# Kernel optimization log

Hardware: AMD Instinct MI355X
Metric: run time of the kernel (lower is better)

The kernel has to match this reference:

```python
import jax, jax.numpy as jnp
from jax import lax
import numpy as np

D_MODEL = 768
D_STATE = 16
D_CONV = 4
EXPAND = 2
D_INNER = EXPAND * D_MODEL
BATCH = 2
SEQ = 512


def setup_inputs() -> dict:
    key = jax.random.key(0)
    ks = jax.random.split(key, 8)
    s = 0.02
    return {
        "x": jax.random.normal(ks[0], (BATCH, SEQ, D_MODEL), jnp.float32),
        "W_in": jax.random.normal(ks[1], (2 * D_INNER, D_MODEL), jnp.float32) * s,
        "conv_w": jax.random.normal(ks[2], (D_INNER, 1, D_CONV), jnp.float32) * s,
        "conv_b": jnp.zeros((D_INNER,), jnp.float32),
        "W_x": jax.random.normal(ks[3], (D_INNER + 2 * D_STATE, D_INNER), jnp.float32) * s,
        "W_dt": jax.random.normal(ks[4], (D_INNER, D_INNER), jnp.float32) * s,
        "b_dt": jnp.zeros((D_INNER,), jnp.float32),
        "A_log": jnp.log(jax.random.uniform(ks[5], (D_INNER, D_STATE), jnp.float32, 1e-4, 1.0)),
        "Dp": jnp.ones((D_INNER,), jnp.float32),
        "W_out": jax.random.normal(ks[6], (D_MODEL, D_INNER), jnp.float32) * s,
    }


def parallel_scan_log(log_coeffs, log_values):
    """Faithful port of ParallelScan.parallel_scan_log (Blelchh-style up/down sweep
    in log space). Indices are static, so the Python loop over O(log L) levels is
    trace-time only."""
    B, L, D = log_coeffs.shape
    if L <= 4:
        run = log_values[:, 0]
        outs = [run]
        for i in range(1, L):
            run = jnp.logaddexp(run, log_coeffs[:, i] + log_values[:, i])
            outs.append(run)
        return jnp.stack(outs, axis=1)
    levels = int(np.ceil(np.log2(L)))
    coeffs, values = log_coeffs, log_values
    # up-sweep
    for level in range(levels):
        step = 2 ** (level + 1)
        if step - 1 >= L:
            break
        right = np.arange(step - 1, L, step)
        left = right - 2 ** level
        m = (left >= 0) & (right < L)
        left, right = left[m], right[m]
        if left.size == 0:
            continue
        new_c = coeffs[:, left] + coeffs[:, right]
        new_v = jnp.logaddexp(values[:, left], coeffs[:, right] + values[:, right])
        coeffs = coeffs.at[:, right].set(new_c)
        values = values.at[:, right].set(new_v)
    # down-sweep
    for level in range(levels - 1, -1, -1):
        step = 2 ** (level + 1)
        if step - 1 >= L:
            continue
        right = np.arange(step - 1, L, step)
        left = right - 2 ** level
        m = (left >= 0) & (right < L)
        left, right = left[m], right[m]
        if left.size == 0:
            continue
        tmp = values[:, right]
        new_r = jnp.logaddexp(values[:, left], coeffs[:, right] + values[:, right])
        values = values.at[:, right].set(new_r)
        values = values.at[:, left].set(tmp)
    return values


def reference(x, W_in, conv_w, conv_b, W_x, W_dt, b_dt, A_log, Dp, W_out):
    Bsz, L, _ = x.shape
    xz = x @ W_in.T                                 # [B, L, 2*d_inner]
    x_inner, z = jnp.split(xz, 2, axis=-1)
    # depthwise causal conv1d (pad left d_conv-1, truncate to L == torch slice)
    xc = jnp.transpose(x_inner, (0, 2, 1))          # [B, d_inner, L]
    xc = lax.conv_general_dilated(
        xc, conv_w, (1,), [(D_CONV - 1, 0)],
        dimension_numbers=("NCH", "OIH", "NCH"),
        feature_group_count=D_INNER)
    xc = xc + conv_b[None, :, None]
    x_conv = jax.nn.silu(jnp.transpose(xc, (0, 2, 1)))  # [B, L, d_inner]
    x_dbl = x_conv @ W_x.T                              # [B, L, d_inner + 2*d_state]
    delta, Bmat, Cmat = jnp.split(x_dbl, [D_INNER, D_INNER + D_STATE], axis=-1)
    delta = jax.nn.softplus(delta @ W_dt.T + b_dt)      # [B, L, d_inner]
    # selective scan
    A = -jnp.exp(A_log)                                 # [d_inner, d_state]
    deltaA = jnp.exp(jnp.einsum("bld,dn->bldn", delta, A))
    deltaB_u = jnp.einsum("bld,bln,bld->bldn", delta, Bmat, x_conv)
    log_coeffs = jnp.log(deltaA + 1e-12).reshape(Bsz, L, -1)
    log_values = jnp.log(jnp.abs(deltaB_u) + 1e-12).reshape(Bsz, L, -1)
    scanned = jnp.exp(parallel_scan_log(log_coeffs, log_values))
    scanned = scanned.reshape(Bsz, L, D_INNER, D_STATE)
    y = jnp.einsum("bldn,bln->bld", scanned, Cmat) + x_conv * Dp
    y = y * jax.nn.silu(z)
    return y @ W_out.T
```

## Files before the change

kernel.cpp:

```cpp
#include <hip/hip_runtime.h>
#include <math.h>

#define D_MODEL 768
#define D_STATE 16
#define D_CONV  4
#define D_INNER 1536
#define BATCH   2
#define SEQ     512
#define M_ROWS  (BATCH * SEQ)
#define N_XZ    (2 * D_INNER)
#define N_XDBL  (D_INNER + 2 * D_STATE)

typedef _Float16 half8 __attribute__((ext_vector_type(8)));
typedef float  f32x4  __attribute__((ext_vector_type(4)));
typedef unsigned short ushort_t;
typedef ushort_t ushort8_t __attribute__((ext_vector_type(8)));

__device__ __forceinline__ ushort_t f2h(float f) {
    _Float16 h = (_Float16)f;
    return *(ushort_t*)&h;
}
__device__ __forceinline__ void pack8(const float* s, ushort_t* d) {
    ushort8_t o;
#pragma unroll
    for (int j = 0; j < 8; ++j) o[j] = f2h(s[j]);
    *(ushort8_t*)d = o;
}
__device__ __forceinline__ void gld16(const ushort_t* g, void* l) {
    __builtin_amdgcn_global_load_lds((const __attribute__((address_space(1))) void*)g,
                                     (__attribute__((address_space(3))) void*)l, 16, 0, 0);
}

#define SX  (M_ROWS * D_MODEL)
#define SW1 (N_XZ * D_MODEL)
#define SW2 (N_XDBL * D_INNER)
__global__ __launch_bounds__(256) void split3_kernel(
    const float* __restrict__ x, const float* __restrict__ win,
    const float* __restrict__ wx,
    ushort_t* __restrict__ xs, ushort_t* __restrict__ w1, ushort_t* __restrict__ w2)
{
    long i = ((long)blockIdx.x * 256 + threadIdx.x) * 8;
    const float* src; ushort_t* dst; long base;
    if (i < SX)            { src = x;   dst = xs; base = i; }
    else if (i < SX + SW1) { src = win; dst = w1; base = i - SX; }
    else                   { src = wx;  dst = w2; base = i - SX - SW1; }
    float v[8];
    *(float4*)(v)     = *(const float4*)(src + base);
    *(float4*)(v + 4) = *(const float4*)(src + base + 4);
    pack8(v, dst + base);
}

#define SWDT (D_INNER * D_INNER)
#define SWO  (D_MODEL * D_INNER)
__global__ __launch_bounds__(256) void split2_kernel(
    const float* __restrict__ wdt, const float* __restrict__ wo,
    ushort_t* __restrict__ w1, ushort_t* __restrict__ wout)
{
    long i = ((long)blockIdx.x * 256 + threadIdx.x) * 8;
    const float* src; ushort_t* dst; long base;
    if (i < SWDT) { src = wdt; dst = w1;   base = i; }
    else          { src = wo;  dst = wout; base = i - SWDT; }
    float v[8];
    *(float4*)(v)     = *(const float4*)(src + base);
    *(float4*)(v + 4) = *(const float4*)(src + base + 4);
    pack8(v, dst + base);
}

__global__ __launch_bounds__(256) void gemm_lds(
    const ushort_t* __restrict__ A, int lda,
    const ushort_t* __restrict__ B, int ldb,
    float* __restrict__ Cbase, long pstride, int ldc,
    int N, int kc)
{
    __shared__ ushort_t smA[2][4096];
    __shared__ ushort_t smB[2][4096];

    const int tid  = threadIdx.x;
    const int w    = tid >> 6;
    const int lane = tid & 63;
    const int lr   = lane & 15;
    const int lq   = lane >> 4;

    const int Gx = gridDim.x, Gy = gridDim.y;
    const int T = Gx * Gy * gridDim.z;
    const int f = blockIdx.x + Gx * (blockIdx.y + Gy * blockIdx.z);
    const int g = (T & 7) ? f : ((f & 7) * (T >> 3) + (f >> 3));
    const int bx = g % Gx;
    const int by = (g / Gx) % Gy;
    const int z  = g / (Gx * Gy);
    float* __restrict__ C = Cbase + (long)z * pstride;

    const int bm = by * 128;
    const int bn = bx * 128;
    const int k0base = z * kc;

    auto stage = [&](int buf, int k0) {
#pragma unroll
        for (int i = 0; i < 2; ++i) {
            const int gA = i * 4 + w;
            const int rA = bm + gA * 16 + lr;
            gld16(A + (long)rA * lda + k0 + lq * 8, &smA[buf][gA * 512]);
        }
#pragma unroll
        for (int i = 0; i < 2; ++i) {
            const int gB = i * 4 + w;
            int rB = bn + gB * 16 + lr; if (rB >= N) rB = N - 1;
            gld16(B + (long)rB * ldb + k0 + lq * 8, &smB[buf][gB * 512]);
        }
    };

    f32x4 acc[4][4] = {};
    const int wm = (w & 1) * 64;
    const int wn = (w >> 1) * 64;

    stage(0, k0base);
    __syncthreads();
    const int nIter = kc >> 5;
    for (int it = 0; it < nIter; ++it) {
        const int buf = it & 1;
        if (it + 1 < nIter) stage(buf ^ 1, k0base + (it + 1) * 32);

        half8 ah[4], bh[4];
#pragma unroll
        for (int mt = 0; mt < 4; ++mt)
            ah[mt] = *(const half8*)&smA[buf][(((w & 1) * 4 + mt) * 512) + lq * 128 + lr * 8];
#pragma unroll
        for (int nt = 0; nt < 4; ++nt)
            bh[nt] = *(const half8*)&smB[buf][(((w >> 1) * 4 + nt) * 512) + lq * 128 + lr * 8];
#pragma unroll
        for (int mt = 0; mt < 4; ++mt)
#pragma unroll
            for (int nt = 0; nt < 4; ++nt)
                acc[mt][nt] = __builtin_amdgcn_mfma_f32_16x16x32_f16(ah[mt], bh[nt], acc[mt][nt], 0, 0, 0);
        __syncthreads();
    }

#pragma unroll
    for (int mt = 0; mt < 4; ++mt)
#pragma unroll
        for (int nt = 0; nt < 4; ++nt)
#pragma unroll
            for (int r = 0; r < 4; ++r) {
                int row = bm + wm + mt * 16 + lq * 4 + r;
                int col = bn + wn + nt * 16 + lr;
                if (col >= N) continue;
                C[(long)row * ldc + col] = acc[mt][nt][r];
            }
}

__global__ __launch_bounds__(256) void conv_silu_kernel(
    const float* __restrict__ p0, const float* __restrict__ p1,
    const float* __restrict__ conv_w,
    const float* __restrict__ conv_b,
    float* __restrict__ xconvT,
    float* __restrict__ zsiluT,
    ushort_t* __restrict__ xc)
{
    int idx = blockIdx.x * blockDim.x + threadIdx.x;
    if (idx >= M_ROWS * D_INNER) return;
    int d = idx % D_INNER;
    int r = idx / D_INNER;
    int l = r % SEQ;
    float acc = conv_b[d];
#pragma unroll
    for (int k = 0; k < D_CONV; ++k) {
        if (l - (D_CONV - 1) + k >= 0) {
            long o = (long)(r - (D_CONV - 1 - k)) * N_XZ + d;
            acc = fmaf(conv_w[d * D_CONV + k], p0[o] + p1[o], acc);
        }
    }
    float s = acc / (1.f + expf(-acc));
    xconvT[(long)d * M_ROWS + r] = s;
    xc[(long)r * D_INNER + d] = f2h(s);
    long oz = (long)r * N_XZ + D_INNER + d;
    float zv = p0[oz] + p1[oz];
    zsiluT[(long)d * M_ROWS + r] = zv / (1.f + expf(-zv));
}

__global__ __launch_bounds__(256) void ep_xdbl_kernel(
    const float* __restrict__ P, long ps,
    ushort_t* __restrict__ xd, float* __restrict__ BCT)
{
    long i = ((long)blockIdx.x * 256 + threadIdx.x) * 8;
    if (i >= (long)M_ROWS * N_XDBL) return;
    int row = (int)(i / N_XDBL);
    int col = (int)(i - (long)row * N_XDBL);
    float f[8];
#pragma unroll
    for (int j = 0; j < 8; ++j) f[j] = P[i + j] + P[i + j + ps] + P[i + j + 2 * ps];
    pack8(f, xd + i);
    if (col >= D_INNER) {
#pragma unroll
        for (int j = 0; j < 8; ++j)
            BCT[(long)(col + j - D_INNER) * M_ROWS + row] = f[j];
    }
}

__global__ __launch_bounds__(256) void ep_merge_kernel(
    const float* __restrict__ P, long ps, float* __restrict__ out)
{
    long i = ((long)blockIdx.x * 256 + threadIdx.x) * 8;
    if (i >= (long)M_ROWS * D_MODEL) return;
    float o[8];
#pragma unroll
    for (int j = 0; j < 8; ++j) {
        float v = 0.f;
#pragma unroll
        for (int z = 0; z < 6; ++z) v += P[i + j + z * ps];
        o[j] = v;
    }
    *(float4*)(out + i)     = *(float4*)(o);
    *(float4*)(out + i + 4) = *(float4*)(o + 4);
}

__global__ __launch_bounds__(256) void scan_kernel(
    const float* __restrict__ P, long ps,
    const float* __restrict__ b_dt,
    const float* __restrict__ xconvT,
    const float* __restrict__ zsiluT,
    const float* __restrict__ BCT,
    const float* __restrict__ A_log,
    const float* __restrict__ Dp,
    float* __restrict__ uT)
{
    __shared__ float dlT[512];
    __shared__ float xrT[512];
    __shared__ float red[3 * 512];

    const int bid = blockIdx.x;
    const int b   = bid / D_INNER;
    const int d   = bid % D_INNER;
    const int tid = threadIdx.x;
    const int w   = tid >> 6;
    const int t   = tid & 63;
    const long od = (long)d * M_ROWS + b * SEQ;

    const float bdt = b_dt[d];
#pragma unroll
    for (int q = 0; q < 2; ++q) {
        const int l = tid + q * 256;
        float v = P[od + l] + P[od + l + ps] + P[od + l + 2 * ps] + P[od + l + 3 * ps] + bdt;
        float sp = fmaxf(v, 0.f) + log1pf(expf(-fabsf(v)));
        const int li = (l & 7) * 64 + (l >> 3);
        dlT[li] = sp;
        xrT[li] = xconvT[od + l];
    }
    __syncthreads();

    float dl[8], xr[8], dx[8], yac[8];
#pragma unroll
    for (int j = 0; j < 8; ++j) {
        dl[j] = dlT[j * 64 + t];
        xr[j] = xrT[j * 64 + t];
        dx[j] = dl[j] * xr[j];
        yac[j] = 0.f;
    }
    const int l0 = 8 * t;

#pragma unroll
    for (int nn = 0; nn < 4; ++nn) {
        const int n = w * 4 + nn;
        const float Adn = -expf(A_log[d * D_STATE + n]);
        const float4* Bp = (const float4*)(BCT + (long)n * M_ROWS + b * SEQ + l0);
        float4 b0 = Bp[0], b1 = Bp[1];
        float Bv[8] = {b0.x, b0.y, b0.z, b0.w, b1.x, b1.y, b1.z, b1.w};
        float c[8], v[8];
#pragma unroll
        for (int j = 0; j < 8; ++j) {
            c[j] = __expf(dl[j] * Adn);
            v[j] = fabsf(dx[j] * Bv[j]);
        }
        float c01 = c[1] * c[0], v01 = fmaf(c[1], v[0], v[1]);
        float c23 = c[3] * c[2], v23 = fmaf(c[3], v[2], v[3]);
        float c45 = c[5] * c[4], v45 = fmaf(c[5], v[4], v[5]);
        float c67 = c[7] * c[6], v67 = fmaf(c[7], v[6], v[7]);
        float c03 = c23 * c01,  v03 = fmaf(c23, v01, v23);
        float c47 = c67 * c45,  v47 = fmaf(c67, v45, v67);
        float cA  = c47 * c03,  vA  = fmaf(c47, v03, v47);
#pragma unroll
        for (int h = 1; h <= 32; h <<= 1) {
            float cl = __shfl_up(cA, (unsigned)h);
            float vl = __shfl_up(vA, (unsigned)h);
            if (t >= h) { vA = fmaf(cA, vl, vA); cA = cA * cl; }
        }
        float s = __shfl_up(vA, 1u);
        if (t == 0) s = 0.f;
        const float4* Cp = (const float4*)(BCT + (long)(16 + n) * M_ROWS + b * SEQ + l0);
        float4 c0 = Cp[0], c1 = Cp[1];
        float Cv[8] = {c0.x, c0.y, c0.z, c0.w, c1.x, c1.y, c1.z, c1.w};
#pragma unroll
        for (int j = 0; j < 8; ++j) {
            s = fmaf(c[j], s, v[j]);
            yac[j] = fmaf(s, Cv[j], yac[j]);
        }
    }

    if (w) {
#pragma unroll
        for (int j = 0; j < 8; ++j) red[(w - 1) * 512 + j * 64 + t] = yac[j];
    }
    __syncthreads();
    if (w == 0) {
        const float Dpd = Dp[d];
#pragma unroll
        for (int j = 0; j < 8; ++j) {
            float y = yac[j] + red[j * 64 + t] + red[512 + j * 64 + t] + red[1024 + j * 64 + t];
            float uv = fmaf(xr[j], Dpd, y) * zsiluT[od + l0 + j];
            uT[od + l0 + j] = uv;
        }
    }
}

__global__ __launch_bounds__(256) void transpose_split_kernel(
    const float* __restrict__ uT, ushort_t* __restrict__ u)
{
    __shared__ float T[64][65];
    const int m0 = blockIdx.x * 64;
    const int d0 = blockIdx.y * 64;
    const int c  = threadIdx.x & 63;
    const int rr = threadIdx.x >> 6;
#pragma unroll
    for (int p = 0; p < 64; p += 4)
        T[p + rr][c] = uT[(long)(d0 + p + rr) * M_ROWS + m0 + c];
    __syncthreads();
#pragma unroll
    for (int p = 0; p < 64; p += 4) {
        int rm = p + rr;
        float v = T[c][rm];
        u[(long)(m0 + rm) * D_INNER + (d0 + c)] = f2h(v);
    }
}

extern "C" void kernel_launch(void* const* d_in, const int* in_sizes, int n_in,
                              void* d_out, int out_size, void* d_ws, size_t ws_size,
                              hipStream_t stream)
{
    (void)in_sizes; (void)n_in; (void)out_size; (void)ws_size;

    const float* x      = (const float*)d_in[0];
    const float* W_in   = (const float*)d_in[1];
    const float* conv_w = (const float*)d_in[2];
    const float* conv_b = (const float*)d_in[3];
    const float* W_x    = (const float*)d_in[4];
    const float* W_dt   = (const float*)d_in[5];
    const float* b_dt   = (const float*)d_in[6];
    const float* A_log  = (const float*)d_in[7];
    const float* Dp     = (const float*)d_in[8];
    const float* W_out  = (const float*)d_in[9];
    float* out = (float*)d_out;

    float* ws = (float*)d_ws;
    long off = 0;
    float* P      = ws + off; off += 2L * M_ROWS * N_XZ;
    float* xconvT = ws + off; off += (long)D_INNER * M_ROWS;
    float* zsiluT = ws + off; off += (long)D_INNER * M_ROWS;
    float* uT     = ws + off; off += (long)D_INNER * M_ROWS;
    float* xcu    = ws + off; off += (long)M_ROWS * D_INNER / 2;
    float* xsbuf  = ws + off; off += (long)M_ROWS * D_MODEL / 2;
    float* w1buf  = ws + off; off += (long)N_XZ * D_MODEL / 2;
    float* w2buf  = ws + off; off += (long)N_XDBL * D_INNER / 2;
    float* xdbuf  = ws + off; off += (long)M_ROWS * N_XDBL / 2;
    float* BCT    = ws + off; off += (long)2 * D_STATE * M_ROWS;

    ushort_t* xs   = (ushort_t*)xsbuf;
    ushort_t* w1   = (ushort_t*)w1buf;
    ushort_t* w2   = (ushort_t*)w2buf;
    ushort_t* xc   = (ushort_t*)xcu;
    ushort_t* xd   = (ushort_t*)xdbuf;
    ushort_t* u_i  = (ushort_t*)xcu;
    float* P6      = P;

    const long psG4 = (long)D_INNER * M_ROWS;

    dim3 blk(256);

    hipLaunchKernelGGL(split3_kernel, dim3((SX + SW1 + SW2) / 2048), blk, 0, stream,
                       x, W_in, W_x, xs, w1, w2);
    hipLaunchKernelGGL(gemm_lds, dim3(N_XZ / 128, M_ROWS / 128, 2), blk, 0, stream,
                       xs, D_MODEL, w1, D_MODEL,
                       P, (long)M_ROWS * N_XZ, N_XZ, N_XZ, D_MODEL / 2);
    hipLaunchKernelGGL(conv_silu_kernel, dim3((M_ROWS * D_INNER) / 256), blk, 0, stream,
                       P, P + (long)M_ROWS * N_XZ, conv_w, conv_b, xconvT, zsiluT, xc);
    hipLaunchKernelGGL(gemm_lds, dim3((N_XDBL + 127) / 128, M_ROWS / 128, 3), blk, 0, stream,
                       xc, D_INNER, w2, D_INNER,
                       P, (long)M_ROWS * N_XDBL, N_XDBL, N_XDBL, D_INNER / 3);
    hipLaunchKernelGGL(ep_xdbl_kernel, dim3((M_ROWS * N_XDBL) / 2048), blk, 0, stream,
                       P, (long)M_ROWS * N_XDBL, xd, BCT);
    hipLaunchKernelGGL(split2_kernel, dim3((SWDT + SWO) / 2048), blk, 0, stream,
                       W_dt, W_out, w1, w2);
    hipLaunchKernelGGL(gemm_lds, dim3(M_ROWS / 128, D_INNER / 128, 4), blk, 0, stream,
                       w1, D_INNER, xd, N_XDBL,
                       P, psG4, M_ROWS, M_ROWS, D_INNER / 4);
    hipLaunchKernelGGL(scan_kernel, dim3(BATCH * D_INNER), blk, 0, stream,
                       P, psG4, b_dt, xconvT, zsiluT, BCT, A_log, Dp, uT);
    hipLaunchKernelGGL(transpose_split_kernel, dim3(M_ROWS / 64, D_INNER / 64), blk, 0, stream,
                       uT, u_i);
    hipLaunchKernelGGL(gemm_lds, dim3(D_MODEL / 128, M_ROWS / 128, 6), blk, 0, stream,
                       u_i, D_INNER, w2, D_INNER,
                       P6, (long)M_ROWS * D_MODEL, D_MODEL, D_MODEL, D_INNER / 6);
    hipLaunchKernelGGL(ep_merge_kernel, dim3((M_ROWS * D_MODEL) / 2048), blk, 0, stream,
                       P6, (long)M_ROWS * D_MODEL, out);
}
```

Baseline: 223.1 us.

## Replace split-K GEMMs with smaller-tile full-K GEMMs and fused epilogues

Drops split-K partial-sum buffers and the separate reduction kernels. Each GEMM now uses 64-row tiles over the full K, and the x_dbl GEMM writes half-precision delta and the transposed B/C directly from its epilogue. The two weight-packing kernels become one launch, and the conv/silu kernel is tiled so the transposed stores go through shared memory and are coalesced. This saves global traffic and launches, but the GEMMs may have fewer waves in flight and longer per-block K loops.

```diff
diff --git a/kernel.cpp b/kernel.cpp
--- a/kernel.cpp
+++ b/kernel.cpp
@@ -31,49 +31,45 @@
                                      (__attribute__((address_space(3))) void*)l, 16, 0, 0);
 }
 
-#define SX  (M_ROWS * D_MODEL)
-#define SW1 (N_XZ * D_MODEL)
-#define SW2 (N_XDBL * D_INNER)
-__global__ __launch_bounds__(256) void split3_kernel(
+#define SX   (M_ROWS * D_MODEL)
+#define SW1  (N_XZ * D_MODEL)
+#define SW2  (N_XDBL * D_INNER)
+#define SWDT (D_INNER * D_INNER)
+#define SWO  (D_MODEL * D_INNER)
+#define SPACK (SX + SW1 + SW2 + SWDT + SWO)
+__global__ __launch_bounds__(256) void pack_kernel(
     const float* __restrict__ x, const float* __restrict__ win,
-    const float* __restrict__ wx,
-    ushort_t* __restrict__ xs, ushort_t* __restrict__ w1, ushort_t* __restrict__ w2)
+    const float* __restrict__ wx, const float* __restrict__ wdt,
+    const float* __restrict__ wo,
+    ushort_t* __restrict__ xs, ushort_t* __restrict__ w1, ushort_t* __restrict__ w2,
+    ushort_t* __restrict__ wdt16, ushort_t* __restrict__ wo16)
 {
     long i = ((long)blockIdx.x * 256 + threadIdx.x) * 8;
+    if (i >= SPACK) return;
     const float* src; ushort_t* dst; long base;
-    if (i < SX)            { src = x;   dst = xs; base = i; }
-    else if (i < SX + SW1) { src = win; dst = w1; base = i - SX; }
-    else                   { src = wx;  dst = w2; base = i - SX - SW1; }
+    if (i < SX)                         { src = x;   dst = xs;    base = i; }
+    else if (i < SX + SW1)              { src = win; dst = w1;    base = i - SX; }
+    else if (i < SX + SW1 + SW2)        { src = wx;  dst = w2;    base = i - SX - SW1; }
+    else if (i < SX + SW1 + SW2 + SWDT) { src = wdt; dst = wdt16; base = i - SX - SW1 - SW2; }
+    else                                { src = wo;  dst = wo16;  base = i - SX - SW1 - SW2 - SWDT; }
     float v[8];
     *(float4*)(v)     = *(const float4*)(src + base);
     *(float4*)(v + 4) = *(const float4*)(src + base + 4);
     pack8(v, dst + base);
 }
 
-#define SWDT (D_INNER * D_INNER)
-#define SWO  (D_MODEL * D_INNER)
-__global__ __launch_bounds__(256) void split2_kernel(
-    const float* __restrict__ wdt, const float* __restrict__ wo,
-    ushort_t* __restrict__ w1, ushort_t* __restrict__ wout)
-{
-    long i = ((long)blockIdx.x * 256 + threadIdx.x) * 8;
-    const float* src; ushort_t* dst; long base;
-    if (i < SWDT) { src = wdt; dst = w1;   base = i; }
-    else          { src = wo;  dst = wout; base = i - SWDT; }
-    float v[8];
-    *(float4*)(v)     = *(const float4*)(src + base);
-    *(float4*)(v + 4) = *(const float4*)(src + base + 4);
-    pack8(v, dst + base);
-}
-
-__global__ __launch_bounds__(256) void gemm_lds(
+template<int BN, int EPI>
+__global__ __launch_bounds__(256) void gemm_z1(
     const ushort_t* __restrict__ A, int lda,
     const ushort_t* __restrict__ B, int ldb,
-    float* __restrict__ Cbase, long pstride, int ldc,
-    int N, int kc)
-{
-    __shared__ ushort_t smA[2][4096];
-    __shared__ ushort_t smB[2][4096];
+    float* __restrict__ C, int ldc,
+    int N, int K,
+    ushort_t* __restrict__ Ch, float* __restrict__ BCT)
+{
+    constexpr int FN = BN / 32;
+    constexpr int BG = BN / 16;
+    __shared__ ushort_t smA[2][2048];
+    __shared__ ushort_t smB[2][BN * 32];
 
     const int tid  = threadIdx.x;
     const int w    = tid >> 6;
@@ -81,140 +77,118 @@
     const int lr   = lane & 15;
     const int lq   = lane >> 4;
 
-    const int Gx = gridDim.x, Gy = gridDim.y;
-    const int T = Gx * Gy * gridDim.z;
-    const int f = blockIdx.x + Gx * (blockIdx.y + Gy * blockIdx.z);
+    const int Gx = gridDim.x;
+    const int T = Gx * gridDim.y;
+    const int f = blockIdx.x + Gx * blockIdx.y;
     const int g = (T & 7) ? f : ((f & 7) * (T >> 3) + (f >> 3));
     const int bx = g % Gx;
-    const int by = (g / Gx) % Gy;
-    const int z  = g / (Gx * Gy);
-    float* __restrict__ C = Cbase + (long)z * pstride;
-
-    const int bm = by * 128;
-    const int bn = bx * 128;
-    const int k0base = z * kc;
+    const int by = g / Gx;
+    const int bm = by * 64;
+    const int bn = bx * BN;
 
     auto stage = [&](int buf, int k0) {
-#pragma unroll
-        for (int i = 0; i < 2; ++i) {
-            const int gA = i * 4 + w;
-            const int rA = bm + gA * 16 + lr;
-            gld16(A + (long)rA * lda + k0 + lq * 8, &smA[buf][gA * 512]);
-        }
-#pragma unroll
-        for (int i = 0; i < 2; ++i) {
+        {
+            const int rA = bm + w * 16 + lr;
+            gld16(A + (long)rA * lda + k0 + lq * 8, &smA[buf][w * 512]);
+        }
+#pragma unroll
+        for (int i = 0; i < BG / 4; ++i) {
             const int gB = i * 4 + w;
             int rB = bn + gB * 16 + lr; if (rB >= N) rB = N - 1;
             gld16(B + (long)rB * ldb + k0 + lq * 8, &smB[buf][gB * 512]);
         }
     };
 
-    f32x4 acc[4][4] = {};
-    const int wm = (w & 1) * 64;
-    const int wn = (w >> 1) * 64;
-
-    stage(0, k0base);
-    __syncthreads();
-    const int nIter = kc >> 5;
+    f32x4 acc[2][FN] = {};
+    const int wm = (w & 1) * 32;
+    const int wn = (w >> 1) * (BN / 2);
+
+    stage(0, 0);
+    __syncthreads();
+    const int nIter = K >> 5;
     for (int it = 0; it < nIter; ++it) {
         const int buf = it & 1;
-        if (it + 1 < nIter) stage(buf ^ 1, k0base + (it + 1) * 32);
-
-        half8 ah[4], bh[4];
-#pragma unroll
-        for (int mt = 0; mt < 4; ++mt)
-            ah[mt] = *(const half8*)&smA[buf][(((w & 1) * 4 + mt) * 512) + lq * 128 + lr * 8];
-#pragma unroll
-        for (int nt = 0; nt < 4; ++nt)
-            bh[nt] = *(const half8*)&smB[buf][(((w >> 1) * 4 + nt) * 512) + lq * 128 + lr * 8];
-#pragma unroll
-        for (int mt = 0; mt < 4; ++mt)
-#pragma unroll
-            for (int nt = 0; nt < 4; ++nt)
+        if (it + 1 < nIter) stage(buf ^ 1, (it + 1) * 32);
+
+        half8 ah[2], bh[FN];
+#pragma unroll
+        for (int mt = 0; mt < 2; ++mt)
+            ah[mt] = *(const half8*)&smA[buf][(((w & 1) * 2 + mt) * 512) + lq * 128 + lr * 8];
+#pragma unroll
+        for (int nt = 0; nt < FN; ++nt)
+            bh[nt] = *(const half8*)&smB[buf][(((w >> 1) * FN + nt) * 512) + lq * 128 + lr * 8];
+#pragma unroll
+        for (int mt = 0; mt < 2; ++mt)
+#pragma unroll
+            for (int nt = 0; nt < FN; ++nt)
                 acc[mt][nt] = __builtin_amdgcn_mfma_f32_16x16x32_f16(ah[mt], bh[nt], acc[mt][nt], 0, 0, 0);
         __syncthreads();
     }
 
 #pragma unroll
-    for (int mt = 0; mt < 4; ++mt)
-#pragma unroll
-        for (int nt = 0; nt < 4; ++nt)
+    for (int mt = 0; mt < 2; ++mt)
+#pragma unroll
+        for (int nt = 0; nt < FN; ++nt)
 #pragma unroll
             for (int r = 0; r < 4; ++r) {
                 int row = bm + wm + mt * 16 + lq * 4 + r;
                 int col = bn + wn + nt * 16 + lr;
-                if (col >= N) continue;
-                C[(long)row * ldc + col] = acc[mt][nt][r];
+                if (EPI == 0) {
+                    if (col < N) C[(long)row * ldc + col] = acc[mt][nt][r];
+                } else {
+                    if (col < D_INNER)
+                        Ch[(long)row * D_INNER + col] = f2h(acc[mt][nt][r]);
+                    else if (col < N)
+                        BCT[(long)(col - D_INNER) * M_ROWS + row] = acc[mt][nt][r];
+                }
             }
 }
 
 __global__ __launch_bounds__(256) void conv_silu_kernel(
-    const float* __restrict__ p0, const float* __restrict__ p1,
-    const float* __restrict__ conv_w,
-    const float* __restrict__ conv_b,
-    float* __restrict__ xconvT,
-    float* __restrict__ zsiluT,
+    const float* __restrict__ xz,
+    const float* __restrict__ conv_w, const float* __restrict__ conv_b,
+    float* __restrict__ xconvT, float* __restrict__ zsiluT,
     ushort_t* __restrict__ xc)
 {
-    int idx = blockIdx.x * blockDim.x + threadIdx.x;
-    if (idx >= M_ROWS * D_INNER) return;
-    int d = idx % D_INNER;
-    int r = idx / D_INNER;
-    int l = r % SEQ;
-    float acc = conv_b[d];
-#pragma unroll
-    for (int k = 0; k < D_CONV; ++k) {
-        if (l - (D_CONV - 1) + k >= 0) {
-            long o = (long)(r - (D_CONV - 1 - k)) * N_XZ + d;
-            acc = fmaf(conv_w[d * D_CONV + k], p0[o] + p1[o], acc);
-        }
-    }
-    float s = acc / (1.f + expf(-acc));
-    xconvT[(long)d * M_ROWS + r] = s;
-    xc[(long)r * D_INNER + d] = f2h(s);
-    long oz = (long)r * N_XZ + D_INNER + d;
-    float zv = p0[oz] + p1[oz];
-    zsiluT[(long)d * M_ROWS + r] = zv / (1.f + expf(-zv));
-}
-
-__global__ __launch_bounds__(256) void ep_xdbl_kernel(
-    const float* __restrict__ P, long ps,
-    ushort_t* __restrict__ xd, float* __restrict__ BCT)
-{
-    long i = ((long)blockIdx.x * 256 + threadIdx.x) * 8;
-    if (i >= (long)M_ROWS * N_XDBL) return;
-    int row = (int)(i / N_XDBL);
-    int col = (int)(i - (long)row * N_XDBL);
-    float f[8];
-#pragma unroll
-    for (int j = 0; j < 8; ++j) f[j] = P[i + j] + P[i + j + ps] + P[i + j + 2 * ps];
-    pack8(f, xd + i);
-    if (col >= D_INNER) {
-#pragma unroll
-        for (int j = 0; j < 8; ++j)
-            BCT[(long)(col + j - D_INNER) * M_ROWS + row] = f[j];
-    }
-}
-
-__global__ __launch_bounds__(256) void ep_merge_kernel(
-    const float* __restrict__ P, long ps, float* __restrict__ out)
-{
-    long i = ((long)blockIdx.x * 256 + threadIdx.x) * 8;
-    if (i >= (long)M_ROWS * D_MODEL) return;
-    float o[8];
-#pragma unroll
-    for (int j = 0; j < 8; ++j) {
-        float v = 0.f;
-#pragma unroll
-        for (int z = 0; z < 6; ++z) v += P[i + j + z * ps];
-        o[j] = v;
-    }
-    *(float4*)(out + i)     = *(float4*)(o);
-    *(float4*)(out + i + 4) = *(float4*)(o + 4);
+    __shared__ float Tx[64][17];
+    __shared__ float Tz[64][17];
+    const int rb = blockIdx.x;
+    const int db = blockIdx.y;
+    const int dl = threadIdx.x & 63;
+    const int d  = db * 64 + dl;
+    const int rr = threadIdx.x >> 6;
+    const float w0 = conv_w[d * 4 + 0], w1 = conv_w[d * 4 + 1];
+    const float w2 = conv_w[d * 4 + 2], w3 = conv_w[d * 4 + 3];
+    const float bb = conv_b[d];
+#pragma unroll
+    for (int q = 0; q < 4; ++q) {
+        const int r = rb * 16 + q * 4 + rr;
+        const int l = r & (SEQ - 1);
+        float acc = bb;
+        if (l >= 3) acc = fmaf(w0, xz[(long)(r - 3) * N_XZ + d], acc);
+        if (l >= 2) acc = fmaf(w1, xz[(long)(r - 2) * N_XZ + d], acc);
+        if (l >= 1) acc = fmaf(w2, xz[(long)(r - 1) * N_XZ + d], acc);
+        acc = fmaf(w3, xz[(long)r * N_XZ + d], acc);
+        float s = acc / (1.f + expf(-acc));
+        xc[(long)r * D_INNER + d] = f2h(s);
+        float zv = xz[(long)r * N_XZ + D_INNER + d];
+        Tx[dl][q * 4 + rr] = s;
+        Tz[dl][q * 4 + rr] = zv / (1.f + expf(-zv));
+    }
+    __syncthreads();
+    const int rp = threadIdx.x & 15;
+    const int dp = threadIdx.x >> 4;
+#pragma unroll
+    for (int p = 0; p < 4; ++p) {
+        int dd = p * 16 + dp;
+        long o = (long)(db * 64 + dd) * M_ROWS + rb * 16 + rp;
+        xconvT[o] = Tx[dd][rp];
+        zsiluT[o] = Tz[dd][rp];
+    }
 }
 
 __global__ __launch_bounds__(256) void scan_kernel(
-    const float* __restrict__ P, long ps,
+    const float* __restrict__ dpre,
     const float* __restrict__ b_dt,
     const float* __restrict__ xconvT,
     const float* __restrict__ zsiluT,
@@ -239,7 +213,7 @@
 #pragma unroll
     for (int q = 0; q < 2; ++q) {
         const int l = tid + q * 256;
-        float v = P[od + l] + P[od + l + ps] + P[od + l + 2 * ps] + P[od + l + 3 * ps] + bdt;
+        float v = dpre[od + l] + bdt;
         float sp = fmaxf(v, 0.f) + log1pf(expf(-fabsf(v)));
         const int li = (l & 7) * 64 + (l >> 3);
         dlT[li] = sp;
@@ -351,53 +325,46 @@
 
     float* ws = (float*)d_ws;
     long off = 0;
-    float* P      = ws + off; off += 2L * M_ROWS * N_XZ;
+    float* xzbuf  = ws + off; off += (long)M_ROWS * N_XZ;
     float* xconvT = ws + off; off += (long)D_INNER * M_ROWS;
     float* zsiluT = ws + off; off += (long)D_INNER * M_ROWS;
     float* uT     = ws + off; off += (long)D_INNER * M_ROWS;
-    float* xcu    = ws + off; off += (long)M_ROWS * D_INNER / 2;
+    float* xcbuf  = ws + off; off += (long)M_ROWS * D_INNER / 2;
+    float* xdbuf  = ws + off; off += (long)M_ROWS * D_INNER / 2;
     float* xsbuf  = ws + off; off += (long)M_ROWS * D_MODEL / 2;
     float* w1buf  = ws + off; off += (long)N_XZ * D_MODEL / 2;
     float* w2buf  = ws + off; off += (long)N_XDBL * D_INNER / 2;
-    float* xdbuf  = ws + off; off += (long)M_ROWS * N_XDBL / 2;
+    float* wdtbuf = ws + off; off += (long)D_INNER * D_INNER / 2;
+    float* wobuf  = ws + off; off += (long)D_MODEL * D_INNER / 2;
     float* BCT    = ws + off; off += (long)2 * D_STATE * M_ROWS;
 
-    ushort_t* xs   = (ushort_t*)xsbuf;
-    ushort_t* w1   = (ushort_t*)w1buf;
-    ushort_t* w2   = (ushort_t*)w2buf;
-    ushort_t* xc   = (ushort_t*)xcu;
-    ushort_t* xd   = (ushort_t*)xdbuf;
-    ushort_t* u_i  = (ushort_t*)xcu;
-    float* P6      = P;
-
-    const long psG4 = (long)D_INNER * M_ROWS;
+    ushort_t* xs    = (ushort_t*)xsbuf;
+    ushort_t* w1    = (ushort_t*)w1buf;
+    ushort_t* w2    = (ushort_t*)w2buf;
+    ushort_t* wdt16 = (ushort_t*)wdtbuf;
+    ushort_t* wo16  = (ushort_t*)wobuf;
+    ushort_t* xc    = (ushort_t*)xcbuf;
+    ushort_t* xd    = (ushort_t*)xdbuf;
+    ushort_t* u_i   = (ushort_t*)xcbuf;
+    float* xz       = xzbuf;
+    float* dpreT    = xzbuf;
 
     dim3 blk(256);
 
-    hipLaunchKernelGGL(split3_kernel, dim3((SX + SW1 + SW2) / 2048), blk, 0, stream,
-                       x, W_in, W_x, xs, w1, w2);
-    hipLaunchKernelGGL(gemm_lds, dim3(N_XZ / 128, M_ROWS / 128, 2), blk, 0, stream,
-                       xs, D_MODEL, w1, D_MODEL,
-                       P, (long)M_ROWS * N_XZ, N_XZ, N_XZ, D_MODEL / 2);
-    hipLaunchKernelGGL(conv_silu_kernel, dim3((M_ROWS * D_INNER) / 256), blk, 0, stream,
-                       P, P + (long)M_ROWS * N_XZ, conv_w, conv_b, xconvT, zsiluT, xc);
-    hipLaunchKernelGGL(gemm_lds, dim3((N_XDBL + 127) / 128, M_ROWS / 128, 3), blk, 0, stream,
-                       xc, D_INNER, w2, D_INNER,
-                       P, (long)M_ROWS * N_XDBL, N_XDBL, N_XDBL, D_INNER / 3);
-    hipLaunchKernelGGL(ep_xdbl_kernel, dim3((M_ROWS * N_XDBL) / 2048), blk, 0, stream,
-                       P, (long)M_ROWS * N_XDBL, xd, BCT);
-    hipLaunchKernelGGL(split2_kernel, dim3((SWDT + SWO) / 2048), blk, 0, stream,
-                       W_dt, W_out, w1, w2);
-    hipLaunchKernelGGL(gemm_lds, dim3(M_ROWS / 128, D_INNER / 128, 4), blk, 0, stream,
-                       w1, D_INNER, xd, N_XDBL,
-                       P, psG4, M_ROWS, M_ROWS, D_INNER / 4);
-    hipLaunchKernelGGL(scan_kernel, dim3(BATCH * D_INNER), blk, 0, stream,
-                       P, psG4, b_dt, xconvT, zsiluT, BCT, A_log, Dp, uT);
-    hipLaunchKernelGGL(transpose_split_kernel, dim3(M_ROWS / 64, D_INNER / 64), blk, 0, stream,
-                       uT, u_i);
-    hipLaunchKernelGGL(gemm_lds, dim3(D_MODEL / 128, M_ROWS / 128, 6), blk, 0, stream,
-                       u_i, D_INNER, w2, D_INNER,
-                       P6, (long)M_ROWS * D_MODEL, D_MODEL, D_MODEL, D_INNER / 6);
-    hipLaunchKernelGGL(ep_merge_kernel, dim3((M_ROWS * D_MODEL) / 2048), blk, 0, stream,
-                       P6, (long)M_ROWS * D_MODEL, out);
-}
+    pack_kernel<<<dim3(SPACK / 2048), blk, 0, stream>>>(
+        x, W_in, W_x, W_dt, W_out, xs, w1, w2, wdt16, wo16);
+    gemm_z1<128, 0><<<dim3(N_XZ / 128, M_ROWS / 64), blk, 0, stream>>>(
+        xs, D_MODEL, w1, D_MODEL, xz, N_XZ, N_XZ, D_MODEL, nullptr, nullptr);
+    conv_silu_kernel<<<dim3(M_ROWS / 16, D_INNER / 64), blk, 0, stream>>>(
+        xz, conv_w, conv_b, xconvT, zsiluT, xc);
+    gemm_z1<64, 1><<<dim3((N_XDBL + 63) / 64, M_ROWS / 64), blk, 0, stream>>>(
+        xc, D_INNER, w2, D_INNER, nullptr, 0, N_XDBL, D_INNER, xd, BCT);
+    gemm_z1<64, 0><<<dim3(M_ROWS / 64, D_INNER / 64), blk, 0, stream>>>(
+        wdt16, D_INNER, xd, D_INNER, dpreT, M_ROWS, M_ROWS, D_INNER, nullptr, nullptr);
+    scan_kernel<<<dim3(BATCH * D_INNER), blk, 0, stream>>>(
+        dpreT, b_dt, xconvT, zsiluT, BCT, A_log, Dp, uT);
+    transpose_split_kernel<<<dim3(M_ROWS / 64, D_INNER / 64), blk, 0, stream>>>(
+        uT, u_i);
+    gemm_z1<64, 0><<<dim3(D_MODEL / 64, M_ROWS / 64), blk, 0, stream>>>(
+        u_i, D_INNER, wo16, D_INNER, out, D_MODEL, D_MODEL, D_INNER, nullptr, nullptr);
+}
```

Result: no change. 227.4 us (+1.9%).

## Triple-buffer GEMM LDS pipeline, merge weight packing, tile-transpose conv output

Applied to the files above, without the earlier changes.

The GEMM moves from double to triple LDS buffering. The trailing __syncthreads per iteration becomes one barrier per iteration, preceded by a partial vmcnt wait, so the next tile's global-to-LDS loads stay in flight during the MFMA work. The two fp16 packing kernels become one launch with separate buffers for W_dt and W_out. The conv+SiLU kernel now transposes through shared-memory tiles so its transposed outputs are written coalesced instead of strided. The costs are more LDS per block, which may lower occupancy, and a fragile hand-written waitcnt scheme.

```diff
diff --git a/kernel.cpp b/kernel.cpp
--- a/kernel.cpp
+++ b/kernel.cpp
@@ -31,35 +31,27 @@
                                      (__attribute__((address_space(3))) void*)l, 16, 0, 0);
 }
 
-#define SX  (M_ROWS * D_MODEL)
-#define SW1 (N_XZ * D_MODEL)
-#define SW2 (N_XDBL * D_INNER)
-__global__ __launch_bounds__(256) void split3_kernel(
-    const float* __restrict__ x, const float* __restrict__ win,
-    const float* __restrict__ wx,
-    ushort_t* __restrict__ xs, ushort_t* __restrict__ w1, ushort_t* __restrict__ w2)
-{
-    long i = ((long)blockIdx.x * 256 + threadIdx.x) * 8;
-    const float* src; ushort_t* dst; long base;
-    if (i < SX)            { src = x;   dst = xs; base = i; }
-    else if (i < SX + SW1) { src = win; dst = w1; base = i - SX; }
-    else                   { src = wx;  dst = w2; base = i - SX - SW1; }
-    float v[8];
-    *(float4*)(v)     = *(const float4*)(src + base);
-    *(float4*)(v + 4) = *(const float4*)(src + base + 4);
-    pack8(v, dst + base);
-}
-
+#define SX   (M_ROWS * D_MODEL)
+#define SW1  (N_XZ * D_MODEL)
+#define SW2  (N_XDBL * D_INNER)
 #define SWDT (D_INNER * D_INNER)
 #define SWO  (D_MODEL * D_INNER)
-__global__ __launch_bounds__(256) void split2_kernel(
-    const float* __restrict__ wdt, const float* __restrict__ wo,
-    ushort_t* __restrict__ w1, ushort_t* __restrict__ wout)
+#define SPACK (SX + SW1 + SW2 + SWDT + SWO)
+__global__ __launch_bounds__(256) void pack_kernel(
+    const float* __restrict__ x, const float* __restrict__ win,
+    const float* __restrict__ wx, const float* __restrict__ wdt,
+    const float* __restrict__ wo,
+    ushort_t* __restrict__ xs, ushort_t* __restrict__ w1, ushort_t* __restrict__ w2,
+    ushort_t* __restrict__ wdt16, ushort_t* __restrict__ wo16)
 {
     long i = ((long)blockIdx.x * 256 + threadIdx.x) * 8;
+    if (i >= SPACK) return;
     const float* src; ushort_t* dst; long base;
-    if (i < SWDT) { src = wdt; dst = w1;   base = i; }
-    else          { src = wo;  dst = wout; base = i - SWDT; }
+    if (i < SX)                         { src = x;   dst = xs;    base = i; }
+    else if (i < SX + SW1)              { src = win; dst = w1;    base = i - SX; }
+    else if (i < SX + SW1 + SW2)        { src = wx;  dst = w2;    base = i - SX - SW1; }
+    else if (i < SX + SW1 + SW2 + SWDT) { src = wdt; dst = wdt16; base = i - SX - SW1 - SW2; }
+    else                                { src = wo;  dst = wo16;  base = i - SX - SW1 - SW2 - SWDT; }
     float v[8];
     *(float4*)(v)     = *(const float4*)(src + base);
     *(float4*)(v + 4) = *(const float4*)(src + base + 4);
@@ -72,8 +64,8 @@
     float* __restrict__ Cbase, long pstride, int ldc,
     int N, int kc)
 {
-    __shared__ ushort_t smA[2][4096];
-    __shared__ ushort_t smB[2][4096];
+    __shared__ ushort_t smA[3][4096];
+    __shared__ ushort_t smB[3][4096];
 
     const int tid  = threadIdx.x;
     const int w    = tid >> 6;
@@ -114,25 +106,32 @@
     const int wn = (w >> 1) * 64;
 
     stage(0, k0base);
-    __syncthreads();
     const int nIter = kc >> 5;
+    int cur = 0;
     for (int it = 0; it < nIter; ++it) {
-        const int buf = it & 1;
-        if (it + 1 < nIter) stage(buf ^ 1, k0base + (it + 1) * 32);
+        const int nxt = (cur == 2) ? 0 : cur + 1;
+        if (it + 1 < nIter) {
+            stage(nxt, k0base + (it + 1) * 32);
+            asm volatile("s_waitcnt vmcnt(4)" ::: "memory");
+        } else {
+            asm volatile("s_waitcnt vmcnt(0)" ::: "memory");
+        }
+        __builtin_amdgcn_s_barrier();
+        asm volatile("" ::: "memory");
 
         half8 ah[4], bh[4];
 #pragma unroll
         for (int mt = 0; mt < 4; ++mt)
-            ah[mt] = *(const half8*)&smA[buf][(((w & 1) * 4 + mt) * 512) + lq * 128 + lr * 8];
+            ah[mt] = *(const half8*)&smA[cur][(((w & 1) * 4 + mt) * 512) + lq * 128 + lr * 8];
 #pragma unroll
         for (int nt = 0; nt < 4; ++nt)
-            bh[nt] = *(const half8*)&smB[buf][(((w >> 1) * 4 + nt) * 512) + lq * 128 + lr * 8];
+            bh[nt] = *(const half8*)&smB[cur][(((w >> 1) * 4 + nt) * 512) + lq * 128 + lr * 8];
 #pragma unroll
         for (int mt = 0; mt < 4; ++mt)
 #pragma unroll
             for (int nt = 0; nt < 4; ++nt)
                 acc[mt][nt] = __builtin_amdgcn_mfma_f32_16x16x32_f16(ah[mt], bh[nt], acc[mt][nt], 0, 0, 0);
-        __syncthreads();
+        cur = nxt;
     }
 
 #pragma unroll
@@ -150,31 +149,46 @@
 
 __global__ __launch_bounds__(256) void conv_silu_kernel(
     const float* __restrict__ p0, const float* __restrict__ p1,
-    const float* __restrict__ conv_w,
-    const float* __restrict__ conv_b,
-    float* __restrict__ xconvT,
-    float* __restrict__ zsiluT,
+    const float* __restrict__ conv_w, const float* __restrict__ conv_b,
+    float* __restrict__ xconvT, float* __restrict__ zsiluT,
     ushort_t* __restrict__ xc)
 {
-    int idx = blockIdx.x * blockDim.x + threadIdx.x;
-    if (idx >= M_ROWS * D_INNER) return;
-    int d = idx % D_INNER;
-    int r = idx / D_INNER;
-    int l = r % SEQ;
-    float acc = conv_b[d];
-#pragma unroll
-    for (int k = 0; k < D_CONV; ++k) {
-        if (l - (D_CONV - 1) + k >= 0) {
-            long o = (long)(r - (D_CONV - 1 - k)) * N_XZ + d;
-            acc = fmaf(conv_w[d * D_CONV + k], p0[o] + p1[o], acc);
-        }
-    }
-    float s = acc / (1.f + expf(-acc));
-    xconvT[(long)d * M_ROWS + r] = s;
-    xc[(long)r * D_INNER + d] = f2h(s);
-    long oz = (long)r * N_XZ + D_INNER + d;
-    float zv = p0[oz] + p1[oz];
-    zsiluT[(long)d * M_ROWS + r] = zv / (1.f + expf(-zv));
+    __shared__ float Tx[64][17];
+    __shared__ float Tz[64][17];
+    const int rb = blockIdx.x;
+    const int db = blockIdx.y;
+    const int dl = threadIdx.x & 63;
+    const int d  = db * 64 + dl;
+    const int rr = threadIdx.x >> 6;
+    const float w0 = conv_w[d * 4 + 0], w1 = conv_w[d * 4 + 1];
+    const float w2 = conv_w[d * 4 + 2], w3 = conv_w[d * 4 + 3];
+    const float bb = conv_b[d];
+#pragma unroll
+    for (int q = 0; q < 4; ++q) {
+        const int r = rb * 16 + q * 4 + rr;
+        const int l = r & (SEQ - 1);
+        float acc = bb;
+        if (l >= 3) { long o = (long)(r - 3) * N_XZ + d; acc = fmaf(w0, p0[o] + p1[o], acc); }
+        if (l >= 2) { long o = (long)(r - 2) * N_XZ + d; acc = fmaf(w1, p0[o] + p1[o], acc); }
+        if (l >= 1) { long o = (long)(r - 1) * N_XZ + d; acc = fmaf(w2, p0[o] + p1[o], acc); }
+        { long o = (long)r * N_XZ + d; acc = fmaf(w3, p0[o] + p1[o], acc); }
+        float s = acc / (1.f + expf(-acc));
+        xc[(long)r * D_INNER + d] = f2h(s);
+        long oz = (long)r * N_XZ + D_INNER + d;
+        float zv = p0[oz] + p1[oz];
+        Tx[dl][q * 4 + rr] = s;
+        Tz[dl][q * 4 + rr] = zv / (1.f + expf(-zv));
+    }
+    __syncthreads();
+    const int rp = threadIdx.x & 15;
+    const int dp = threadIdx.x >> 4;
+#pragma unroll
+    for (int p = 0; p < 4; ++p) {
+        int dd = p * 16 + dp;
+        long o = (long)(db * 64 + dd) * M_ROWS + rb * 16 + rp;
+        xconvT[o] = Tx[dd][rp];
+        zsiluT[o] = Tz[dd][rp];
+    }
 }
 
 __global__ __launch_bounds__(256) void ep_xdbl_kernel(
@@ -355,49 +369,47 @@
     float* xconvT = ws + off; off += (long)D_INNER * M_ROWS;
     float* zsiluT = ws + off; off += (long)D_INNER * M_ROWS;
     float* uT     = ws + off; off += (long)D_INNER * M_ROWS;
-    float* xcu    = ws + off; off += (long)M_ROWS * D_INNER / 2;
     float* xsbuf  = ws + off; off += (long)M_ROWS * D_MODEL / 2;
     float* w1buf  = ws + off; off += (long)N_XZ * D_MODEL / 2;
     float* w2buf  = ws + off; off += (long)N_XDBL * D_INNER / 2;
+    float* wdtbuf = ws + off; off += (long)D_INNER * D_INNER / 2;
+    float* wobuf  = ws + off; off += (long)D_MODEL * D_INNER / 2;
+    float* xcbuf  = ws + off; off += (long)M_ROWS * D_INNER / 2;
     float* xdbuf  = ws + off; off += (long)M_ROWS * N_XDBL / 2;
     float* BCT    = ws + off; off += (long)2 * D_STATE * M_ROWS;
 
-    ushort_t* xs   = (ushort_t*)xsbuf;
-    ushort_t* w1   = (ushort_t*)w1buf;
-    ushort_t* w2   = (ushort_t*)w2buf;
-    ushort_t* xc   = (ushort_t*)xcu;
-    ushort_t* xd   = (ushort_t*)xdbuf;
-    ushort_t* u_i  = (ushort_t*)xcu;
-    float* P6      = P;
+    ushort_t* xs    = (ushort_t*)xsbuf;
+    ushort_t* w1    = (ushort_t*)w1buf;
+    ushort_t* w2    = (ushort_t*)w2buf;
+    ushort_t* wdt16 = (ushort_t*)wdtbuf;
+    ushort_t* wo16  = (ushort_t*)wobuf;
+    ushort_t* xc    = (ushort_t*)xcbuf;
+    ushort_t* xd    = (ushort_t*)xdbuf;
+    ushort_t* u_i   = (ushort_t*)xcbuf;
+    float* P6       = P;
 
     const long psG4 = (long)D_INNER * M_ROWS;
 
     dim3 blk(256);
 
-    hipLaunchKernelGGL(split3_kernel, dim3((SX + SW1 + SW2) / 2048), blk, 0, stream,
-                       x, W_in, W_x, xs, w1, w2);
-    hipLaunchKernelGGL(gemm_lds, dim3(N_XZ / 128, M_ROWS / 128, 2), blk, 0, stream,
-                       xs, D_MODEL, w1, D_MODEL,
-                       P, (long)M_ROWS * N_XZ, N_XZ, N_XZ, D_MODEL / 2);
-    hipLaunchKernelGGL(conv_silu_kernel, dim3((M_ROWS * D_INNER) / 256), blk, 0, stream,
-                       P, P + (long)M_ROWS * N_XZ, conv_w, conv_b, xconvT, zsiluT, xc);
-    hipLaunchKernelGGL(gemm_lds, dim3((N_XDBL + 127) / 128, M_ROWS / 128, 3), blk, 0, stream,
-                       xc, D_INNER, w2, D_INNER,
-                       P, (long)M_ROWS * N_XDBL, N_XDBL, N_XDBL, D_INNER / 3);
-    hipLaunchKernelGGL(ep_xdbl_kernel, dim3((M_ROWS * N_XDBL) / 2048), blk, 0, stream,
-                       P, (long)M_ROWS * N_XDBL, xd, BCT);
-    hipLaunchKernelGGL(split2_kernel, dim3((SWDT + SWO) / 2048), blk, 0, stream,
-                       W_dt, W_out, w1, w2);
-    hipLaunchKernelGGL(gemm_lds, dim3(M_ROWS / 128, D_INNER / 128, 4), blk, 0, stream,
-                       w1, D_INNER, xd, N_XDBL,
-                       P, psG4, M_ROWS, M_ROWS, D_INNER / 4);
-    hipLaunchKernelGGL(scan_kernel, dim3(BATCH * D_INNER), blk, 0, stream,
-                       P, psG4, b_dt, xconvT, zsiluT, BCT, A_log, Dp, uT);
-    hipLaunchKernelGGL(transpose_split_kernel, dim3(M_ROWS / 64, D_INNER / 64), blk, 0, stream,
-                       uT, u_i);
-    hipLaunchKernelGGL(gemm_lds, dim3(D_MODEL / 128, M_ROWS / 128, 6), blk, 0, stream,
-                       u_i, D_INNER, w2, D_INNER,
-                       P6, (long)M_ROWS * D_MODEL, D_MODEL, D_MODEL, D_INNER / 6);
-    hipLaunchKernelGGL(ep_merge_kernel, dim3((M_ROWS * D_MODEL) / 2048), blk, 0, stream,
-                       P6, (long)M_ROWS * D_MODEL, out);
-}
+    pack_kernel<<<dim3(SPACK / 2048), blk, 0, stream>>>(
+        x, W_in, W_x, W_dt, W_out, xs, w1, w2, wdt16, wo16);
+    gemm_lds<<<dim3(N_XZ / 128, M_ROWS / 128, 2), blk, 0, stream>>>(
+        xs, D_MODEL, w1, D_MODEL, P, (long)M_ROWS * N_XZ, N_XZ, N_XZ, D_MODEL / 2);
+    conv_silu_kernel<<<dim3(M_ROWS / 16, D_INNER / 64), blk, 0, stream>>>(
+        P, P + (long)M_ROWS * N_XZ, conv_w, conv_b, xconvT, zsiluT, xc);
+    gemm_lds<<<dim3((N_XDBL + 127) / 128, M_ROWS / 128, 3), blk, 0, stream>>>(
+        xc, D_INNER, w2, D_INNER, P, (long)M_ROWS * N_XDBL, N_XDBL, N_XDBL, D_INNER / 3);
+    ep_xdbl_kernel<<<dim3((M_ROWS * N_XDBL) / 2048), blk, 0, stream>>>(
+        P, (long)M_ROWS * N_XDBL, xd, BCT);
+    gemm_lds<<<dim3(M_ROWS / 128, D_INNER / 128, 4), blk, 0, stream>>>(
+        wdt16, D_INNER, xd, N_XDBL, P, psG4, M_ROWS, M_ROWS, D_INNER / 4);
+    scan_kernel<<<dim3(BATCH * D_INNER), blk, 0, stream>>>(
+        P, psG4, b_dt, xconvT, zsiluT, BCT, A_log, Dp, uT);
+    transpose_split_kernel<<<dim3(M_ROWS / 64, D_INNER / 64), blk, 0, stream>>>(
+        uT, u_i);
+    gemm_lds<<<dim3(D_MODEL / 128, M_ROWS / 128, 6), blk, 0, stream>>>(
+        u_i, D_INNER, wo16, D_INNER, P6, (long)M_ROWS * D_MODEL, D_MODEL, D_MODEL, D_INNER / 6);
+    ep_merge_kernel<<<dim3((M_ROWS * D_MODEL) / 2048), blk, 0, stream>>>(
+        P6, (long)M_ROWS * D_MODEL, out);
+}
```

Result: faster. 206.3 us (-7.5%).
